# Kernel optimization log

Measured on AMD Instinct MI355X. Metric: run time of the kernel, lower is better.

## Reference

```python
import jax, jax.numpy as jnp
import numpy as np

# Model dims (match init_kwargs)
H = 16        # num query heads
HKV = 4       # num key/value heads
D = 128       # head dim
HID = H * D   # hidden size = 2048
W = 4         # ring world size; we simulate rank W-1 (sees all kv shards)
SL = 2048     # local (per-rank) sequence length


def _block_attn(q, kb, vb, scale, causal):
    # q: [B,H,Sl,D], kb/vb: [B,H,Sl,D]
    S = jnp.einsum('bhqd,bhkd->bhqk', q, kb) * scale
    if causal:
        mask = jnp.triu(jnp.ones((q.shape[2], kb.shape[2]), dtype=bool), k=1)
        S = jnp.where(mask[None, None], -jnp.inf, S)
    S_max = jnp.max(S, axis=-1, keepdims=True)
    exp_S = jnp.exp(S - S_max)
    exp_sum = jnp.sum(exp_S, axis=-1, keepdims=True)
    lse = jnp.log(exp_sum) + S_max            # [B,H,Sl,1]
    O = jnp.einsum('bhqk,bhkd->bhqd', exp_S / exp_sum, vb)
    return O, lse


def _ring_attention_fwd(x_q, x_kv, Wq, Wk, Wv, Wo):
    B, Sl, hid = x_q.shape
    n_rep = H // HKV
    scale = 1.0 / np.sqrt(D).astype(np.float32)

    q = (x_q @ Wq.T).reshape(B, Sl, H, D).transpose(0, 2, 1, 3)          # [B,H,Sl,D]
    k = (x_kv @ Wk.T).reshape(B, -1, HKV, D).transpose(0, 2, 1, 3)       # [B,Hkv,Stot,D]
    v = (x_kv @ Wv.T).reshape(B, -1, HKV, D).transpose(0, 2, 1, 3)
    # repeat_kv (GQA)
    k = jnp.repeat(k, n_rep, axis=1)                                     # [B,H,Stot,D]
    v = jnp.repeat(v, n_rep, axis=1)
    # split kv into W ring shards along sequence
    kb = k.reshape(B, H, W, Sl, D)
    vb = v.reshape(B, H, W, Sl, D)

    out, lse = None, None
    rank = W - 1
    for step in range(W):  # fixed small ring loop
        blk = rank - step  # shard held at this ring step (own shard first)
        bo, blse = _block_attn(q, kb[:, :, blk], vb[:, :, blk], scale, causal=(step == 0))
        if out is None:
            out, lse = bo, blse
        else:
            # online merge (matches update_out_and_lse)
            out = out - jax.nn.sigmoid(blse - lse) * (out - bo)
            lse = lse - jax.nn.log_sigmoid(lse - blse)

    out = out.transpose(0, 2, 1, 3).reshape(B, Sl, H * D)
    return out @ Wo.T


def setup_inputs() -> dict:
    key = jax.random.key(0)
    ks = jax.random.split(key, 6)
    s = 0.02
    return {
        'x_q': jax.random.normal(ks[0], (1, SL, HID), dtype=jnp.float32),
        'x_kv': jax.random.normal(ks[1], (1, W * SL, HID), dtype=jnp.float32),
        'Wq': jax.random.normal(ks[2], (HID, HID), dtype=jnp.float32) * s,
        'Wk': jax.random.normal(ks[3], (HKV * D, HID), dtype=jnp.float32) * s,
        'Wv': jax.random.normal(ks[4], (HKV * D, HID), dtype=jnp.float32) * s,
        'Wo': jax.random.normal(ks[5], (HID, HID), dtype=jnp.float32) * s,
    }


def reference(x_q, x_kv, Wq, Wk, Wv, Wo):
    return _ring_attention_fwd(x_q, x_kv, Wq, Wk, Wv, Wo)
```

## Files before the change

### kernel.cpp

```cpp
#include <hip/hip_runtime.h>
#include <stdint.h>

typedef unsigned short u16;
typedef short bf16x8 __attribute__((ext_vector_type(8)));
typedef float f32x4 __attribute__((ext_vector_type(4)));
typedef float f32x16 __attribute__((ext_vector_type(16)));

#define MFMA16(a, b, c) __builtin_amdgcn_mfma_f32_16x16x32_bf16(a, b, c, 0, 0, 0)
#define MFMA32(a, b, c) __builtin_amdgcn_mfma_f32_32x32x16_bf16(a, b, c, 0, 0, 0)

__device__ __forceinline__ void ld_lds16(const void* g, void* l) {
  __builtin_amdgcn_global_load_lds(
      (const __attribute__((address_space(1))) void*)(uint64_t)(uintptr_t)g,
      (__attribute__((address_space(3))) void*)(uint32_t)(uintptr_t)l,
      16, 0, 0);
}

__device__ __forceinline__ u16 f32_to_bf16(float f) {
  uint32_t u = __float_as_uint(f);
  return (u16)((u + 0x7FFFu + ((u >> 16) & 1u)) >> 16);
}

__device__ __forceinline__ uint32_t cvt_pk_bf16(float a, float b) {
  uint32_t r;
  asm("v_cvt_pk_bf16_f32 %0, %1, %2" : "=v"(r) : "v"(a), "v"(b));
  return r;
}

__device__ __forceinline__ void perm_swap(uint32_t& x, uint32_t& y) {
  asm volatile("v_permlane32_swap_b32 %0, %1" : "+v"(x), "+v"(y));
}

__global__ void cvt_all(const float* __restrict__ xq, const float* __restrict__ xkv,
                        const float* __restrict__ Wq, const float* __restrict__ Wk,
                        const float* __restrict__ Wv, const float* __restrict__ Wo,
                        u16* __restrict__ xq_b, u16* __restrict__ xkv_b,
                        u16* __restrict__ wq_b, u16* __restrict__ wk_b,
                        u16* __restrict__ wv_b, u16* __restrict__ wo_b) {
  const int M4 = 1 << 20;
  const int total = 7 * M4 + (M4 >> 1);
  int i = blockIdx.x * blockDim.x + threadIdx.x;
  int stride = gridDim.x * blockDim.x;
  for (; i < total; i += stride) {
    const float* src;
    u16* dst;
    int off;
    if (i < M4)                         { src = xq;  dst = xq_b;  off = i; }
    else if (i < 5 * M4)                { src = xkv; dst = xkv_b; off = i - M4; }
    else if (i < 6 * M4)                { src = Wq;  dst = wq_b;  off = i - 5 * M4; }
    else if (i < 6 * M4 + (M4 >> 2))    { src = Wk;  dst = wk_b;  off = i - 6 * M4; }
    else if (i < 6 * M4 + (M4 >> 1))    { src = Wv;  dst = wv_b;  off = i - 6 * M4 - (M4 >> 2); }
    else                                { src = Wo;  dst = wo_b;  off = i - 6 * M4 - (M4 >> 1); }
    float4 v = reinterpret_cast<const float4*>(src)[off];
    ushort4 o;
    o.x = f32_to_bf16(v.x); o.y = f32_to_bf16(v.y);
    o.z = f32_to_bf16(v.z); o.w = f32_to_bf16(v.w);
    reinterpret_cast<ushort4*>(dst)[off] = o;
  }
}

__device__ __forceinline__ void gemm_body(const u16* __restrict__ A,
                                          const u16* __restrict__ B,
                                          void* __restrict__ Cv, int M, int N,
                                          int K, float alpha, int bx, int by,
                                          int outf32, u16* lA, u16* lB) {
  const int tid = threadIdx.x;
  const int lane = tid & 63;
  const int w = tid >> 6;
  const int c = lane & 15, g = lane >> 4;
  const int wm = (w & 1) * 64, wn = (w >> 1) * 32;
  const int m0 = by * 128, n0 = bx * 64;
  const int sr = tid >> 3, sc = tid & 7;

  f32x4 acc[4][2] = {};

  for (int k0 = 0; k0 < K; k0 += 64) {
    __syncthreads();
#pragma unroll
    for (int p = 0; p < 4; ++p) {
      int row = p * 32 + sr;
      int gc = sc ^ (row & 7);
      ld_lds16(A + (size_t)(m0 + row) * K + k0 + gc * 8, &lA[row * 64 + sc * 8]);
    }
#pragma unroll
    for (int p = 0; p < 2; ++p) {
      int idx = p * 256 + tid;
      int row = idx >> 3, cc = idx & 7;
      int gc = cc ^ (row & 7);
      ld_lds16(B + (size_t)(n0 + row) * K + k0 + gc * 8, &lB[row * 64 + cc * 8]);
    }
    __syncthreads();
#pragma unroll
    for (int kc = 0; kc < 2; ++kc) {
      bf16x8 a[4], b[2];
#pragma unroll
      for (int t = 0; t < 4; ++t) {
        int row = wm + t * 16 + c;
        int ch = (g + 4 * kc) ^ (row & 7);
        a[t] = *(const bf16x8*)&lA[row * 64 + ch * 8];
      }
#pragma unroll
      for (int t = 0; t < 2; ++t) {
        int row = wn + t * 16 + c;
        int ch = (g + 4 * kc) ^ (row & 7);
        b[t] = *(const bf16x8*)&lB[row * 64 + ch * 8];
      }
#pragma unroll
      for (int i = 0; i < 4; ++i)
#pragma unroll
        for (int j = 0; j < 2; ++j)
          acc[i][j] = MFMA16(a[i], b[j], acc[i][j]);
    }
  }

#pragma unroll
  for (int i = 0; i < 4; ++i)
#pragma unroll
    for (int j = 0; j < 2; ++j)
#pragma unroll
      for (int r = 0; r < 4; ++r) {
        int mm = m0 + wm + i * 16 + g * 4 + r;
        int nn = n0 + wn + j * 16 + c;
        float v = acc[i][j][r] * alpha;
        if (outf32)
          ((float*)Cv)[(size_t)mm * N + nn] = v;
        else
          ((u16*)Cv)[(size_t)mm * N + nn] = f32_to_bf16(v);
      }
}

__global__ __launch_bounds__(256, 4)
void gemm3(const u16* __restrict__ xq_b, const u16* __restrict__ wq_b,
           u16* __restrict__ Qb, const u16* __restrict__ xkv_b,
           const u16* __restrict__ wk_b, u16* __restrict__ Kb,
           const u16* __restrict__ wv_b, u16* __restrict__ VTb, float qscale) {
  __shared__ u16 lA[128 * 64];
  __shared__ u16 lB[64 * 64];
  int b = blockIdx.x;
  if (b < 512) {
    gemm_body(xq_b, wq_b, Qb, 2048, 2048, 2048, qscale, b & 31, b >> 5, 0, lA, lB);
  } else if (b < 1024) {
    b -= 512;
    gemm_body(xkv_b, wk_b, Kb, 8192, 512, 2048, 1.0f, b & 7, b >> 3, 0, lA, lB);
  } else {
    b -= 1024;
    gemm_body(wv_b, xkv_b, VTb, 512, 8192, 2048, 1.0f, b & 127, b >> 7, 0, lA, lB);
  }
}

__global__ __launch_bounds__(256, 4)
void gemm_out(const u16* __restrict__ A, const u16* __restrict__ B,
              float* __restrict__ Cv) {
  __shared__ u16 lA[128 * 64];
  __shared__ u16 lB[64 * 64];
  gemm_body(A, B, Cv, 2048, 2048, 2048, 1.0f, blockIdx.x, blockIdx.y, 1, lA, lB);
}

__global__ __launch_bounds__(256, 2)
void attn_kernel(const u16* __restrict__ Q, const u16* __restrict__ Kg,
                 const u16* __restrict__ VT, float* __restrict__ Opart,
                 float* __restrict__ mlp) {
  __shared__ u16 lK[2][64 * 128];
  __shared__ u16 lV[2][128 * 64];

  const int tid = threadIdx.x;
  const int w = tid >> 6, lane = tid & 63;
  const int ql = lane & 31, hi = lane >> 5;
  const int bx = blockIdx.x;
  const int h = bx & 15, kvs = bx >> 8;
  const int qbr = (bx >> 4) & 15;
  const int qb = kvs ? qbr : 15 - qbr;
  const int hk = h >> 2;
  const int i0 = qb * 128;
  const int q0 = i0 + w * 32;

  const int nt = ((i0 + 6271) >> 6) + 1;
  const int nth = nt >> 1;
  const int t0 = kvs ? nth : 0;
  const int ntt = (kvs ? nt : nth) - t0;

  bf16x8 qf[8];
#pragma unroll
  for (int kc = 0; kc < 8; ++kc)
    qf[kc] = *(const bf16x8*)&Q[(size_t)(q0 + ql) * 2048 + h * 128 + kc * 16 + hi * 8];

  f32x16 a[4] = {};
  float ls = 0.f;

  auto stage = [&](int buf, int t) {
    const int j0 = t << 6;
#pragma unroll
    for (int p = 0; p < 4; ++p) {
      int idx = p * 256 + tid;
      int row = idx >> 4, cc = idx & 15;
      int gc = cc ^ (row & 15);
      ld_lds16(Kg + (size_t)(j0 + row) * 512 + hk * 128 + gc * 8,
               &lK[buf][row * 128 + cc * 8]);
    }
#pragma unroll
    for (int p = 0; p < 4; ++p) {
      int idx = p * 256 + tid;
      int row = idx >> 3, cc = idx & 7;
      int gc = cc ^ (row & 7);
      ld_lds16(VT + (size_t)(hk * 128 + row) * 8192 + j0 + gc * 8,
               &lV[buf][row * 64 + cc * 8]);
    }
  };

  stage(0, t0);

  for (int it = 0; it < ntt; ++it) {
    const int curb = it & 1;
    const int j0 = (t0 + it) << 6;
    if (it + 1 < ntt) {
      stage(curb ^ 1, t0 + it + 1);
      asm volatile("s_waitcnt vmcnt(8)" ::: "memory");
    } else {
      asm volatile("s_waitcnt vmcnt(0)" ::: "memory");
    }
    __builtin_amdgcn_s_barrier();

    f32x16 s0 = {}, s1 = {};
    __builtin_amdgcn_s_setprio(1);
#pragma unroll
    for (int kc = 0; kc < 8; ++kc) {
      int ch = kc * 2 + hi;
      bf16x8 kfa = *(const bf16x8*)&lK[curb][ql * 128 + (ch ^ (ql & 15)) * 8];
      bf16x8 kfb = *(const bf16x8*)&lK[curb][(32 + ql) * 128 + (ch ^ (ql & 15)) * 8];
      s0 = MFMA32(kfa, qf[kc], s0);
      s1 = MFMA32(kfb, qf[kc], s1);
    }
    __builtin_amdgcn_s_setprio(0);

    if (j0 + 63 > q0 + 6144) {
#pragma unroll
      for (int r = 0; r < 16; ++r) {
        int jrow = (r & 3) + 8 * (r >> 2) + 4 * hi;
        if (j0 + jrow > q0 + ql + 6144) s0[r] = -1e30f;
        if (j0 + 32 + jrow > q0 + ql + 6144) s1[r] = -1e30f;
      }
    }

    float t0s = 0.f, t1s = 0.f, t2s = 0.f, t3s = 0.f;
#pragma unroll
    for (int r = 0; r < 16; r += 4) {
      s0[r] = exp2f(s0[r]);     t0s += s0[r];
      s0[r + 1] = exp2f(s0[r + 1]); t1s += s0[r + 1];
      s0[r + 2] = exp2f(s0[r + 2]); t2s += s0[r + 2];
      s0[r + 3] = exp2f(s0[r + 3]); t3s += s0[r + 3];
    }
#pragma unroll
    for (int r = 0; r < 16; r += 4) {
      s1[r] = exp2f(s1[r]);     t0s += s1[r];
      s1[r + 1] = exp2f(s1[r + 1]); t1s += s1[r + 1];
      s1[r + 2] = exp2f(s1[r + 2]); t2s += s1[r + 2];
      s1[r + 3] = exp2f(s1[r + 3]); t3s += s1[r + 3];
    }
    float ts = (t0s + t1s) + (t2s + t3s);
    ts += __shfl_xor(ts, 32);
    ls += ts;

    bf16x8 pbf[4];
#pragma unroll
    for (int jt = 0; jt < 2; ++jt) {
      const f32x16& sv = jt ? s1 : s0;
      uint32_t A0 = cvt_pk_bf16(sv[0], sv[1]);
      uint32_t B0 = cvt_pk_bf16(sv[4], sv[5]);
      perm_swap(A0, B0);
      uint32_t A1 = cvt_pk_bf16(sv[2], sv[3]);
      uint32_t B1 = cvt_pk_bf16(sv[6], sv[7]);
      perm_swap(A1, B1);
      uint32_t A2 = cvt_pk_bf16(sv[8], sv[9]);
      uint32_t B2 = cvt_pk_bf16(sv[12], sv[13]);
      perm_swap(A2, B2);
      uint32_t A3 = cvt_pk_bf16(sv[10], sv[11]);
      uint32_t B3 = cvt_pk_bf16(sv[14], sv[15]);
      perm_swap(A3, B3);
      union { uint32_t u[4]; bf16x8 v; } pa, pb;
      pa.u[0] = A0; pa.u[1] = A1; pa.u[2] = B0; pa.u[3] = B1;
      pb.u[0] = A2; pb.u[1] = A3; pb.u[2] = B2; pb.u[3] = B3;
      pbf[2 * jt] = pa.v;
      pbf[2 * jt + 1] = pb.v;
    }

    __builtin_amdgcn_s_setprio(1);
#pragma unroll
    for (int kc = 0; kc < 4; ++kc)
#pragma unroll
      for (int dt = 0; dt < 4; ++dt) {
        int row = dt * 32 + ql;
        int ch = (kc * 2 + hi) ^ (row & 7);
        bf16x8 vf = *(const bf16x8*)&lV[curb][row * 64 + ch * 8];
        a[dt] = MFMA32(pbf[kc], vf, a[dt]);
      }
    __builtin_amdgcn_s_setprio(0);

    __builtin_amdgcn_s_barrier();
  }

  const size_t pbase = ((size_t)(kvs * 16 + h) * 16 + qb);
  float* Op = Opart + pbase * 16384;
  float* mlb = mlp + pbase * 256;
#pragma unroll
  for (int dt = 0; dt < 4; ++dt)
#pragma unroll
    for (int r = 0; r < 16; ++r) {
      int qrow = w * 32 + (r & 3) + 8 * (r >> 2) + 4 * hi;
      Op[(size_t)qrow * 128 + dt * 32 + ql] = a[dt][r];
    }
  if (hi == 0) mlb[128 + w * 32 + ql] = ls;
}

__global__ __launch_bounds__(256)
void attn_merge(const float* __restrict__ Opart, const float* __restrict__ mlp,
                u16* __restrict__ O) {
  const int bx = blockIdx.x;
  const int h = bx >> 4, qb = bx & 15;
  const int q = threadIdx.x & 127, hf = threadIdx.x >> 7;
  const size_t p0 = ((size_t)(0 + h) * 16 + qb);
  const size_t p1 = ((size_t)(16 + h) * 16 + qb);
  float ll0 = mlp[p0 * 256 + 128 + q], ll1 = mlp[p1 * 256 + 128 + q];
  float inv = 1.f / (ll0 + ll1);
  const float* A = Opart + p0 * 16384 + (size_t)q * 128 + hf * 64;
  const float* B = Opart + p1 * 16384 + (size_t)q * 128 + hf * 64;
  u16* out = O + (size_t)(qb * 128 + q) * 2048 + h * 128 + hf * 64;
#pragma unroll
  for (int d = 0; d < 64; d += 4) {
    float4 a = *(const float4*)&A[d];
    float4 b = *(const float4*)&B[d];
    ushort4 o;
    o.x = f32_to_bf16((a.x + b.x) * inv);
    o.y = f32_to_bf16((a.y + b.y) * inv);
    o.z = f32_to_bf16((a.z + b.z) * inv);
    o.w = f32_to_bf16((a.w + b.w) * inv);
    *(ushort4*)&out[d] = o;
  }
}

extern "C" void kernel_launch(void* const* d_in, const int* in_sizes, int n_in,
                              void* d_out, int out_size, void* d_ws, size_t ws_size,
                              hipStream_t stream) {
  (void)in_sizes; (void)n_in; (void)out_size; (void)ws_size;
  const float* xq = (const float*)d_in[0];
  const float* xkv = (const float*)d_in[1];
  const float* Wq = (const float*)d_in[2];
  const float* Wk = (const float*)d_in[3];
  const float* Wv = (const float*)d_in[4];
  const float* Wo = (const float*)d_in[5];

  u16* ws = (u16*)d_ws;
  const size_t M1 = 1024 * 1024;
  u16* xq_b  = ws;
  u16* xkv_b = ws + 4 * M1;
  u16* wq_b  = ws + 20 * M1;
  u16* wk_b  = ws + 24 * M1;
  u16* wv_b  = ws + 25 * M1;
  u16* wo_b  = ws + 26 * M1;
  u16* Qb    = ws + 30 * M1;
  u16* Kb    = ws + 34 * M1;
  u16* VTb   = ws + 38 * M1;
  u16* Ob    = ws + 42 * M1;
  float* Opart = (float*)d_ws;
  float* mlptr = Opart + 8388608;

  cvt_all<<<2048, 256, 0, stream>>>(xq, xkv, Wq, Wk, Wv, Wo,
                                    xq_b, xkv_b, wq_b, wk_b, wv_b, wo_b);

  gemm3<<<1536, 256, 0, stream>>>(xq_b, wq_b, Qb, xkv_b, wk_b, Kb, wv_b, VTb,
                                  0.12752837f);

  attn_kernel<<<512, 256, 0, stream>>>(Qb, Kb, VTb, Opart, mlptr);
  attn_merge<<<256, 256, 0, stream>>>(Opart, mlptr, Ob);

  gemm_out<<<dim3(32, 16), 256, 0, stream>>>(Ob, wo_b, (float*)d_out);
}
```

Before: 296.9 us.

## Split attention KV range three ways and halve the KV tile

The attention kernel now splits each query block's KV range across three blocks instead of two, launching 768 blocks, and the merge kernel sums three partials. The KV tile per iteration shrinks from 64 to 32 rows, and occupancy is raised to 3 blocks per CU. The aim is better load balance and more resident waves across CUs. The cost is more barriers and staging per unit of MFMA work, plus one extra partial buffer to write and read in the merge.

```diff
diff --git a/kernel.cpp b/kernel.cpp
--- a/kernel.cpp
+++ b/kernel.cpp
@@ -156,12 +156,12 @@
   gemm_body(A, B, Cv, 2048, 2048, 2048, 1.0f, blockIdx.x, blockIdx.y, 1, lA, lB);
 }
 
-__global__ __launch_bounds__(256, 2)
+__global__ __launch_bounds__(256, 3)
 void attn_kernel(const u16* __restrict__ Q, const u16* __restrict__ Kg,
                  const u16* __restrict__ VT, float* __restrict__ Opart,
                  float* __restrict__ mlp) {
-  __shared__ u16 lK[2][64 * 128];
-  __shared__ u16 lV[2][128 * 64];
+  __shared__ u16 lK[2][32 * 128];
+  __shared__ u16 lV[2][128 * 32];
 
   const int tid = threadIdx.x;
   const int w = tid >> 6, lane = tid & 63;
@@ -169,15 +169,15 @@
   const int bx = blockIdx.x;
   const int h = bx & 15, kvs = bx >> 8;
   const int qbr = (bx >> 4) & 15;
-  const int qb = kvs ? qbr : 15 - qbr;
+  const int qb = 15 - qbr;
   const int hk = h >> 2;
   const int i0 = qb * 128;
   const int q0 = i0 + w * 32;
 
-  const int nt = ((i0 + 6271) >> 6) + 1;
-  const int nth = nt >> 1;
-  const int t0 = kvs ? nth : 0;
-  const int ntt = (kvs ? nt : nth) - t0;
+  const int nt = (i0 + 6303) >> 5;
+  const int t0 = (nt * kvs) / 3;
+  const int t1 = (nt * (kvs + 1)) / 3;
+  const int ntt = t1 - t0;
 
   bf16x8 qf[8];
 #pragma unroll
@@ -188,9 +188,9 @@
   float ls = 0.f;
 
   auto stage = [&](int buf, int t) {
-    const int j0 = t << 6;
-#pragma unroll
-    for (int p = 0; p < 4; ++p) {
+    const int j0 = t << 5;
+#pragma unroll
+    for (int p = 0; p < 2; ++p) {
       int idx = p * 256 + tid;
       int row = idx >> 4, cc = idx & 15;
       int gc = cc ^ (row & 15);
@@ -198,12 +198,12 @@
                &lK[buf][row * 128 + cc * 8]);
     }
 #pragma unroll
-    for (int p = 0; p < 4; ++p) {
+    for (int p = 0; p < 2; ++p) {
       int idx = p * 256 + tid;
-      int row = idx >> 3, cc = idx & 7;
-      int gc = cc ^ (row & 7);
+      int row = idx >> 2, cc = idx & 3;
+      int gc = cc ^ (row & 3);
       ld_lds16(VT + (size_t)(hk * 128 + row) * 8192 + j0 + gc * 8,
-               &lV[buf][row * 64 + cc * 8]);
+               &lV[buf][row * 32 + cc * 8]);
     }
   };
 
@@ -211,86 +211,74 @@
 
   for (int it = 0; it < ntt; ++it) {
     const int curb = it & 1;
-    const int j0 = (t0 + it) << 6;
+    const int j0 = (t0 + it) << 5;
     if (it + 1 < ntt) {
       stage(curb ^ 1, t0 + it + 1);
-      asm volatile("s_waitcnt vmcnt(8)" ::: "memory");
+      asm volatile("s_waitcnt vmcnt(4)" ::: "memory");
     } else {
       asm volatile("s_waitcnt vmcnt(0)" ::: "memory");
     }
     __builtin_amdgcn_s_barrier();
 
-    f32x16 s0 = {}, s1 = {};
+    f32x16 s = {};
     __builtin_amdgcn_s_setprio(1);
 #pragma unroll
     for (int kc = 0; kc < 8; ++kc) {
       int ch = kc * 2 + hi;
-      bf16x8 kfa = *(const bf16x8*)&lK[curb][ql * 128 + (ch ^ (ql & 15)) * 8];
-      bf16x8 kfb = *(const bf16x8*)&lK[curb][(32 + ql) * 128 + (ch ^ (ql & 15)) * 8];
-      s0 = MFMA32(kfa, qf[kc], s0);
-      s1 = MFMA32(kfb, qf[kc], s1);
+      bf16x8 kf = *(const bf16x8*)&lK[curb][ql * 128 + (ch ^ (ql & 15)) * 8];
+      s = MFMA32(kf, qf[kc], s);
     }
     __builtin_amdgcn_s_setprio(0);
 
-    if (j0 + 63 > q0 + 6144) {
+    if (j0 + 31 > q0 + 6144) {
 #pragma unroll
       for (int r = 0; r < 16; ++r) {
         int jrow = (r & 3) + 8 * (r >> 2) + 4 * hi;
-        if (j0 + jrow > q0 + ql + 6144) s0[r] = -1e30f;
-        if (j0 + 32 + jrow > q0 + ql + 6144) s1[r] = -1e30f;
+        if (j0 + jrow > q0 + ql + 6144) s[r] = -1e30f;
       }
     }
 
     float t0s = 0.f, t1s = 0.f, t2s = 0.f, t3s = 0.f;
 #pragma unroll
     for (int r = 0; r < 16; r += 4) {
-      s0[r] = exp2f(s0[r]);     t0s += s0[r];
-      s0[r + 1] = exp2f(s0[r + 1]); t1s += s0[r + 1];
-      s0[r + 2] = exp2f(s0[r + 2]); t2s += s0[r + 2];
-      s0[r + 3] = exp2f(s0[r + 3]); t3s += s0[r + 3];
-    }
-#pragma unroll
-    for (int r = 0; r < 16; r += 4) {
-      s1[r] = exp2f(s1[r]);     t0s += s1[r];
-      s1[r + 1] = exp2f(s1[r + 1]); t1s += s1[r + 1];
-      s1[r + 2] = exp2f(s1[r + 2]); t2s += s1[r + 2];
-      s1[r + 3] = exp2f(s1[r + 3]); t3s += s1[r + 3];
+      s[r] = exp2f(s[r]);         t0s += s[r];
+      s[r + 1] = exp2f(s[r + 1]); t1s += s[r + 1];
+      s[r + 2] = exp2f(s[r + 2]); t2s += s[r + 2];
+      s[r + 3] = exp2f(s[r + 3]); t3s += s[r + 3];
     }
     float ts = (t0s + t1s) + (t2s + t3s);
     ts += __shfl_xor(ts, 32);
     ls += ts;
 
-    bf16x8 pbf[4];
-#pragma unroll
-    for (int jt = 0; jt < 2; ++jt) {
-      const f32x16& sv = jt ? s1 : s0;
-      uint32_t A0 = cvt_pk_bf16(sv[0], sv[1]);
-      uint32_t B0 = cvt_pk_bf16(sv[4], sv[5]);
+    bf16x8 pbf[2];
+    {
+      uint32_t A0 = cvt_pk_bf16(s[0], s[1]);
+      uint32_t B0 = cvt_pk_bf16(s[4], s[5]);
       perm_swap(A0, B0);
-      uint32_t A1 = cvt_pk_bf16(sv[2], sv[3]);
-      uint32_t B1 = cvt_pk_bf16(sv[6], sv[7]);
+      uint32_t A1 = cvt_pk_bf16(s[2], s[3]);
+      uint32_t B1 = cvt_pk_bf16(s[6], s[7]);
       perm_swap(A1, B1);
-      uint32_t A2 = cvt_pk_bf16(sv[8], sv[9]);
-      uint32_t B2 = cvt_pk_bf16(sv[12], sv[13]);
+      uint32_t A2 = cvt_pk_bf16(s[8], s[9]);
+      uint32_t B2 = cvt_pk_bf16(s[12], s[13]);
       perm_swap(A2, B2);
-      uint32_t A3 = cvt_pk_bf16(sv[10], sv[11]);
-      uint32_t B3 = cvt_pk_bf16(sv[14], sv[15]);
+      uint32_t A3 = cvt_pk_bf16(s[10], s[11]);
+      uint32_t B3 = cvt_pk_bf16(s[14], s[15]);
       perm_swap(A3, B3);
       union { uint32_t u[4]; bf16x8 v; } pa, pb;
       pa.u[0] = A0; pa.u[1] = A1; pa.u[2] = B0; pa.u[3] = B1;
       pb.u[0] = A2; pb.u[1] = A3; pb.u[2] = B2; pb.u[3] = B3;
-      pbf[2 * jt] = pa.v;
-      pbf[2 * jt + 1] = pb.v;
+      pbf[0] = pa.v;
+      pbf[1] = pb.v;
     }
 
     __builtin_amdgcn_s_setprio(1);
 #pragma unroll
-    for (int kc = 0; kc < 4; ++kc)
+    for (int kc = 0; kc < 2; ++kc)
 #pragma unroll
       for (int dt = 0; dt < 4; ++dt) {
         int row = dt * 32 + ql;
-        int ch = (kc * 2 + hi) ^ (row & 7);
-        bf16x8 vf = *(const bf16x8*)&lV[curb][row * 64 + ch * 8];
+        int ch = (kc * 2 + hi) ^ (row & 3);
+        bf16x8 vf = *(const bf16x8*)&lV[curb][row * 32 + ch * 8];
         a[dt] = MFMA32(pbf[kc], vf, a[dt]);
       }
     __builtin_amdgcn_s_setprio(0);
@@ -317,22 +305,30 @@
   const int bx = blockIdx.x;
   const int h = bx >> 4, qb = bx & 15;
   const int q = threadIdx.x & 127, hf = threadIdx.x >> 7;
-  const size_t p0 = ((size_t)(0 + h) * 16 + qb);
-  const size_t p1 = ((size_t)(16 + h) * 16 + qb);
-  float ll0 = mlp[p0 * 256 + 128 + q], ll1 = mlp[p1 * 256 + 128 + q];
-  float inv = 1.f / (ll0 + ll1);
-  const float* A = Opart + p0 * 16384 + (size_t)q * 128 + hf * 64;
-  const float* B = Opart + p1 * 16384 + (size_t)q * 128 + hf * 64;
+
+  float lsum = 0.f;
+#pragma unroll
+  for (int s = 0; s < 3; ++s) {
+    size_t pidx = ((size_t)(s * 16 + h) * 16 + qb);
+    lsum += mlp[pidx * 256 + 128 + q];
+  }
+  float inv = 1.f / lsum;
+
   u16* out = O + (size_t)(qb * 128 + q) * 2048 + h * 128 + hf * 64;
 #pragma unroll
   for (int d = 0; d < 64; d += 4) {
-    float4 a = *(const float4*)&A[d];
-    float4 b = *(const float4*)&B[d];
+    float acc0 = 0.f, acc1 = 0.f, acc2 = 0.f, acc3 = 0.f;
+#pragma unroll
+    for (int s = 0; s < 3; ++s) {
+      size_t pidx = ((size_t)(s * 16 + h) * 16 + qb);
+      float4 v = *(const float4*)&Opart[pidx * 16384 + (size_t)q * 128 + hf * 64 + d];
+      acc0 += v.x; acc1 += v.y; acc2 += v.z; acc3 += v.w;
+    }
     ushort4 o;
-    o.x = f32_to_bf16((a.x + b.x) * inv);
-    o.y = f32_to_bf16((a.y + b.y) * inv);
-    o.z = f32_to_bf16((a.z + b.z) * inv);
-    o.w = f32_to_bf16((a.w + b.w) * inv);
+    o.x = f32_to_bf16(acc0 * inv);
+    o.y = f32_to_bf16(acc1 * inv);
+    o.z = f32_to_bf16(acc2 * inv);
+    o.w = f32_to_bf16(acc3 * inv);
     *(ushort4*)&out[d] = o;
   }
 }
@@ -361,7 +357,7 @@
   u16* VTb   = ws + 38 * M1;
   u16* Ob    = ws + 42 * M1;
   float* Opart = (float*)d_ws;
-  float* mlptr = Opart + 8388608;
+  float* mlptr = Opart + 12582912;
 
   cvt_all<<<2048, 256, 0, stream>>>(xq, xkv, Wq, Wk, Wv, Wo,
                                     xq_b, xkv_b, wq_b, wk_b, wv_b, wo_b);
@@ -369,7 +365,7 @@
   gemm3<<<1536, 256, 0, stream>>>(xq_b, wq_b, Qb, xkv_b, wk_b, Kb, wv_b, VTb,
                                   0.12752837f);
 
-  attn_kernel<<<512, 256, 0, stream>>>(Qb, Kb, VTb, Opart, mlptr);
+  attn_kernel<<<768, 256, 0, stream>>>(Qb, Kb, VTb, Opart, mlptr);
   attn_merge<<<256, 256, 0, stream>>>(Opart, mlptr, Ob);
 
   gemm_out<<<dim3(32, 16), 256, 0, stream>>>(Ob, wo_b, (float*)d_out);
```

After: 321.0 us. +8.1%, slower.
